# Optimization experiments

Hardware: AMD Instinct MI355X
Metric: run time of the kernel (lower is better)

Reference implementation:

```python
import jax, jax.numpy as jnp
import numpy as np

N = 4096      # nodes
IN = 512      # in_features
H = 8         # heads
D = 64        # out_features // heads (out % heads == 0)
EDGE_PROB = 0.01


def setup_inputs() -> dict:
    key = jax.random.key(0)
    kx, ka, kw, ko, kd = jax.random.split(key, 5)
    x = jax.random.normal(kx, (N, IN), dtype=jnp.float32)
    # dense binary adjacency with self-loops (original indexes adj[loc, :] as a mask)
    adj = (jax.random.uniform(ka, (N, N)) < EDGE_PROB).astype(jnp.float32)
    adj = jnp.maximum(adj, jnp.eye(N, dtype=jnp.float32))
    # stacked per-head params (original keeps Python lists of equal-sized heads)
    W = jax.random.normal(kw, (H, IN, D), dtype=jnp.float32) * (1.0 / np.sqrt(IN))
    a_origin = jax.random.normal(ko, (H, D), dtype=jnp.float32) * 0.1
    a_dst = jax.random.normal(kd, (H, D), dtype=jnp.float32) * 0.1
    return {"x": x, "adj": adj, "W": W, "a_origin": a_origin, "a_dst": a_dst}


def reference(x, adj, W, a_origin, a_dst):
    # per-head projection: mx[h] = x @ W[h]  -> [H, N, D]
    mx = jnp.einsum('nf,hfd->hnd', x, W)
    # clacAttn: e_ij = exp(mx_i . a_origin + mx_j . a_dst), masked by adj[i,:], row-normalised
    s_i = jnp.einsum('hnd,hd->hn', mx, a_origin)   # source term (row)
    t_j = jnp.einsum('hnd,hd->hn', mx, a_dst)      # dest term (col)
    logits = s_i[:, :, None] + t_j[:, None, :]     # [H, N, N]
    neg_inf = jnp.finfo(logits.dtype).min
    masked = jnp.where(adj[None] > 0, logits, neg_inf)
    attn = jax.nn.softmax(masked, axis=-1)         # == exp/masked-sum of original
    out_h = jnp.einsum('hij,hjd->hid', attn, mx)   # [H, N, D]
    # hstack over heads -> [N, H*D]
    return jnp.transpose(out_h, (1, 0, 2)).reshape(N, H * D)
```

## Files before the change

kernel.cpp:

```cpp
#include <hip/hip_runtime.h>
#include <hip/hip_bf16.h>

#define N_NODES 4096
#define IN_F    512
#define HEADS   8
#define DH      64
#define HD      512

typedef __bf16 bf16x8 __attribute__((ext_vector_type(8)));
typedef float  f32x4  __attribute__((ext_vector_type(4)));

__device__ __forceinline__ float bf_lo(unsigned u) { return __uint_as_float(u << 16); }
__device__ __forceinline__ float bf_hi(unsigned u) { return __uint_as_float(u & 0xffff0000u); }

#define KP 72

__global__ __launch_bounds__(256, 2) void k1_gemm(const float* __restrict__ X,
                                                  const float* __restrict__ W,
                                                  const float* __restrict__ a_dst,
                                                  __bf16* __restrict__ C,
                                                  float* __restrict__ et) {
    __shared__ __bf16 As[2][64][KP];
    __shared__ __bf16 Bs[2][64][KP];
    __shared__ float  ts[2][64];
    int tid  = threadIdx.x;
    int h    = blockIdx.x & 7;
    int y    = blockIdx.x >> 3;
    int row0 = y * 64, col0 = h * 64;
    int wave = tid >> 6, lane = tid & 63;
    int wm = wave >> 1, wn = wave & 1;
    int lr = lane & 15, kg = lane >> 4;

    f32x4 acc[2][2] = {};

    int sr = tid >> 3, sc = (tid & 7) * 8;
    const float* aptr0 = X + (size_t)(row0 + sr) * IN_F + sc;
    const float* aptr1 = aptr0 + (size_t)32 * IN_F;
    int dcol = tid & 63, fq = (tid >> 6) * 16;
    const float* wptr = W + ((size_t)h * IN_F + fq) * DH + dcol;

    f32x4 pa00 = *(const f32x4*)aptr0, pa01 = *(const f32x4*)(aptr0 + 4);
    f32x4 pa10 = *(const f32x4*)aptr1, pa11 = *(const f32x4*)(aptr1 + 4);
    float wv[16];
    #pragma unroll
    for (int i = 0; i < 16; ++i) wv[i] = wptr[(size_t)i * DH];

    float ad0 = a_dst[h * DH + wn * 32 + lr];
    float ad1 = a_dst[h * DH + wn * 32 + 16 + lr];

    #pragma unroll
    for (int k = 0; k < IN_F / 64; ++k) {
        int cur = k & 1;
        bf16x8 a0 = { (__bf16)pa00[0], (__bf16)pa00[1], (__bf16)pa00[2], (__bf16)pa00[3],
                      (__bf16)pa01[0], (__bf16)pa01[1], (__bf16)pa01[2], (__bf16)pa01[3] };
        bf16x8 a1 = { (__bf16)pa10[0], (__bf16)pa10[1], (__bf16)pa10[2], (__bf16)pa10[3],
                      (__bf16)pa11[0], (__bf16)pa11[1], (__bf16)pa11[2], (__bf16)pa11[3] };
        bf16x8 b0 = { (__bf16)wv[0],  (__bf16)wv[1],  (__bf16)wv[2],  (__bf16)wv[3],
                      (__bf16)wv[4],  (__bf16)wv[5],  (__bf16)wv[6],  (__bf16)wv[7] };
        bf16x8 b1 = { (__bf16)wv[8],  (__bf16)wv[9],  (__bf16)wv[10], (__bf16)wv[11],
                      (__bf16)wv[12], (__bf16)wv[13], (__bf16)wv[14], (__bf16)wv[15] };
        *(bf16x8*)&As[cur][sr][sc]        = a0;
        *(bf16x8*)&As[cur][sr + 32][sc]   = a1;
        *(bf16x8*)&Bs[cur][dcol][fq]      = b0;
        *(bf16x8*)&Bs[cur][dcol][fq + 8]  = b1;
        if (k + 1 < IN_F / 64) {
            int off = (k + 1) * 64;
            pa00 = *(const f32x4*)(aptr0 + off); pa01 = *(const f32x4*)(aptr0 + off + 4);
            pa10 = *(const f32x4*)(aptr1 + off); pa11 = *(const f32x4*)(aptr1 + off + 4);
            const float* wp = wptr + (size_t)off * DH;
            #pragma unroll
            for (int i = 0; i < 16; ++i) wv[i] = wp[(size_t)i * DH];
        }
        __syncthreads();
        #pragma unroll
        for (int kc = 0; kc < 2; ++kc) {
            bf16x8 af0 = *(const bf16x8*)&As[cur][wm * 32 + lr]     [kc * 32 + kg * 8];
            bf16x8 af1 = *(const bf16x8*)&As[cur][wm * 32 + 16 + lr][kc * 32 + kg * 8];
            bf16x8 bf0 = *(const bf16x8*)&Bs[cur][wn * 32 + lr]     [kc * 32 + kg * 8];
            bf16x8 bf1 = *(const bf16x8*)&Bs[cur][wn * 32 + 16 + lr][kc * 32 + kg * 8];
            acc[0][0] = __builtin_amdgcn_mfma_f32_16x16x32_bf16(af0, bf0, acc[0][0], 0, 0, 0);
            acc[0][1] = __builtin_amdgcn_mfma_f32_16x16x32_bf16(af0, bf1, acc[0][1], 0, 0, 0);
            acc[1][0] = __builtin_amdgcn_mfma_f32_16x16x32_bf16(af1, bf0, acc[1][0], 0, 0, 0);
            acc[1][1] = __builtin_amdgcn_mfma_f32_16x16x32_bf16(af1, bf1, acc[1][1], 0, 0, 0);
        }
    }

    #pragma unroll
    for (int mt = 0; mt < 2; ++mt) {
        #pragma unroll
        for (int nt = 0; nt < 2; ++nt) {
            int col = col0 + wn * 32 + nt * 16 + lr;
            #pragma unroll
            for (int r = 0; r < 4; ++r) {
                int row = row0 + wm * 32 + mt * 16 + kg * 4 + r;
                C[(size_t)row * HD + col] = (__bf16)acc[mt][nt][r];
            }
        }
    }
    #pragma unroll
    for (int mt = 0; mt < 2; ++mt) {
        #pragma unroll
        for (int r = 0; r < 4; ++r) {
            float p = ad0 * acc[mt][0][r] + ad1 * acc[mt][1][r];
            p += __shfl_xor(p, 1);
            p += __shfl_xor(p, 2);
            p += __shfl_xor(p, 4);
            p += __shfl_xor(p, 8);
            if (lr == 0) ts[wn][wm * 32 + mt * 16 + kg * 4 + r] = p;
        }
    }
    __syncthreads();
    if (tid < 64) {
        float t = ts[0][tid] + ts[1][tid];
        et[(size_t)(row0 + tid) * HEADS + h] = __expf(t);
    }
}

#define MAXNBR 512
__global__ __launch_bounds__(256) void k3_aggr(const float* __restrict__ adj,
                                               const __bf16* __restrict__ mx,
                                               const float* __restrict__ et,
                                               float* __restrict__ out) {
    __shared__ int   jlist[MAXNBR];
    __shared__ int   cnt;
    __shared__ float red[3][64][9];
    int tid  = threadIdx.x;
    int i    = blockIdx.x;
    int w    = tid >> 6, lane = tid & 63;
    if (tid == 0) cnt = 0;

    const uint4* arow = (const uint4*)(adj + (size_t)i * N_NODES);
    uint4 v0 = arow[tid];
    uint4 v1 = arow[256 + tid];
    uint4 v2 = arow[512 + tid];
    uint4 v3 = arow[768 + tid];
    int n = (v0.x != 0) + (v0.y != 0) + (v0.z != 0) + (v0.w != 0)
          + (v1.x != 0) + (v1.y != 0) + (v1.z != 0) + (v1.w != 0)
          + (v2.x != 0) + (v2.y != 0) + (v2.z != 0) + (v2.w != 0)
          + (v3.x != 0) + (v3.y != 0) + (v3.z != 0) + (v3.w != 0);
    __syncthreads();

    int pre = n;
    #pragma unroll
    for (int dlt = 1; dlt < 64; dlt <<= 1) {
        int t = __shfl_up(pre, dlt, 64);
        if (lane >= dlt) pre += t;
    }
    int wtot = __shfl(pre, 63, 64);
    int base = 0;
    if (lane == 63) base = atomicAdd(&cnt, wtot);
    base = __shfl(base, 63, 64);
    if (base + wtot <= MAXNBR) {
        int p_ = base + pre - n;
        int jb = tid * 4;
        if (v0.x) jlist[p_++] = jb;
        if (v0.y) jlist[p_++] = jb + 1;
        if (v0.z) jlist[p_++] = jb + 2;
        if (v0.w) jlist[p_++] = jb + 3;
        jb += 1024;
        if (v1.x) jlist[p_++] = jb;
        if (v1.y) jlist[p_++] = jb + 1;
        if (v1.z) jlist[p_++] = jb + 2;
        if (v1.w) jlist[p_++] = jb + 3;
        jb += 1024;
        if (v2.x) jlist[p_++] = jb;
        if (v2.y) jlist[p_++] = jb + 1;
        if (v2.z) jlist[p_++] = jb + 2;
        if (v2.w) jlist[p_++] = jb + 3;
        jb += 1024;
        if (v3.x) jlist[p_++] = jb;
        if (v3.y) jlist[p_++] = jb + 1;
        if (v3.z) jlist[p_++] = jb + 2;
        if (v3.w) jlist[p_++] = jb + 3;
    }
    __syncthreads();
    int c = cnt;
    if (c > MAXNBR) c = MAXNBR;

    int h = lane >> 3;
    const uint4* mxv = (const uint4*)mx;
    float acc[8] = {0.f, 0.f, 0.f, 0.f, 0.f, 0.f, 0.f, 0.f};
    float d = 0.f;

    int  k    = w;
    bool more = (k < c);
    int  j    = more ? jlist[k] : 0;
    float e   = 0.f;
    uint4 p   = {0u, 0u, 0u, 0u};
    if (more) {
        e = et[j * HEADS + h];
        p = mxv[(size_t)j * 64 + lane];
    }
    while (more) {
        int  k2   = k + 4;
        bool m2   = (k2 < c);
        int  j2   = m2 ? jlist[k2] : 0;
        float e2  = 0.f;
        uint4 p2  = {0u, 0u, 0u, 0u};
        if (m2) {
            e2 = et[j2 * HEADS + h];
            p2 = mxv[(size_t)j2 * 64 + lane];
        }
        acc[0] += e * bf_lo(p.x);  acc[1] += e * bf_hi(p.x);
        acc[2] += e * bf_lo(p.y);  acc[3] += e * bf_hi(p.y);
        acc[4] += e * bf_lo(p.z);  acc[5] += e * bf_hi(p.z);
        acc[6] += e * bf_lo(p.w);  acc[7] += e * bf_hi(p.w);
        d += e;
        k = k2; more = m2; j = j2; e = e2; p = p2;
    }

    if (w > 0) {
        #pragma unroll
        for (int q = 0; q < 8; ++q) red[w - 1][lane][q] = acc[q];
        red[w - 1][lane][8] = d;
    }
    __syncthreads();
    if (w == 0) {
        #pragma unroll
        for (int g = 0; g < 3; ++g) {
            #pragma unroll
            for (int q = 0; q < 8; ++q) acc[q] += red[g][lane][q];
            d += red[g][lane][8];
        }
        float inv = 1.f / d;
        f32x4 o0 = { acc[0] * inv, acc[1] * inv, acc[2] * inv, acc[3] * inv };
        f32x4 o1 = { acc[4] * inv, acc[5] * inv, acc[6] * inv, acc[7] * inv };
        float* orow = out + (size_t)i * HD + lane * 8;
        *(f32x4*)orow       = o0;
        *(f32x4*)(orow + 4) = o1;
    }
}

extern "C" void kernel_launch(void* const* d_in, const int* in_sizes, int n_in,
                              void* d_out, int out_size, void* d_ws, size_t ws_size,
                              hipStream_t stream) {
    const float* x     = (const float*)d_in[0];
    const float* adj   = (const float*)d_in[1];
    const float* W     = (const float*)d_in[2];
    const float* a_dst = (const float*)d_in[4];
    float* out = (float*)d_out;

    char* ws = (char*)d_ws;
    __bf16* mx = (__bf16*)ws;
    float*  et = (float*)(ws + 4194304);

    k1_gemm<<<dim3(512), dim3(256), 0, stream>>>(x, W, a_dst, mx, et);
    k3_aggr<<<dim3(N_NODES), dim3(256), 0, stream>>>(adj, mx, et, out);
}
```

Baseline: 127.9 us.

## Split adjacency scan into separate kernel and use single-wave gather blocks

```diff
diff --git a/kernel.cpp b/kernel.cpp
--- a/kernel.cpp
+++ b/kernel.cpp
@@ -13,120 +13,16 @@
 __device__ __forceinline__ float bf_lo(unsigned u) { return __uint_as_float(u << 16); }
 __device__ __forceinline__ float bf_hi(unsigned u) { return __uint_as_float(u & 0xffff0000u); }
 
-#define KP 72
-
-__global__ __launch_bounds__(256, 2) void k1_gemm(const float* __restrict__ X,
-                                                  const float* __restrict__ W,
-                                                  const float* __restrict__ a_dst,
-                                                  __bf16* __restrict__ C,
-                                                  float* __restrict__ et) {
-    __shared__ __bf16 As[2][64][KP];
-    __shared__ __bf16 Bs[2][64][KP];
-    __shared__ float  ts[2][64];
-    int tid  = threadIdx.x;
-    int h    = blockIdx.x & 7;
-    int y    = blockIdx.x >> 3;
-    int row0 = y * 64, col0 = h * 64;
-    int wave = tid >> 6, lane = tid & 63;
-    int wm = wave >> 1, wn = wave & 1;
-    int lr = lane & 15, kg = lane >> 4;
-
-    f32x4 acc[2][2] = {};
-
-    int sr = tid >> 3, sc = (tid & 7) * 8;
-    const float* aptr0 = X + (size_t)(row0 + sr) * IN_F + sc;
-    const float* aptr1 = aptr0 + (size_t)32 * IN_F;
-    int dcol = tid & 63, fq = (tid >> 6) * 16;
-    const float* wptr = W + ((size_t)h * IN_F + fq) * DH + dcol;
-
-    f32x4 pa00 = *(const f32x4*)aptr0, pa01 = *(const f32x4*)(aptr0 + 4);
-    f32x4 pa10 = *(const f32x4*)aptr1, pa11 = *(const f32x4*)(aptr1 + 4);
-    float wv[16];
-    #pragma unroll
-    for (int i = 0; i < 16; ++i) wv[i] = wptr[(size_t)i * DH];
-
-    float ad0 = a_dst[h * DH + wn * 32 + lr];
-    float ad1 = a_dst[h * DH + wn * 32 + 16 + lr];
-
-    #pragma unroll
-    for (int k = 0; k < IN_F / 64; ++k) {
-        int cur = k & 1;
-        bf16x8 a0 = { (__bf16)pa00[0], (__bf16)pa00[1], (__bf16)pa00[2], (__bf16)pa00[3],
-                      (__bf16)pa01[0], (__bf16)pa01[1], (__bf16)pa01[2], (__bf16)pa01[3] };
-        bf16x8 a1 = { (__bf16)pa10[0], (__bf16)pa10[1], (__bf16)pa10[2], (__bf16)pa10[3],
-                      (__bf16)pa11[0], (__bf16)pa11[1], (__bf16)pa11[2], (__bf16)pa11[3] };
-        bf16x8 b0 = { (__bf16)wv[0],  (__bf16)wv[1],  (__bf16)wv[2],  (__bf16)wv[3],
-                      (__bf16)wv[4],  (__bf16)wv[5],  (__bf16)wv[6],  (__bf16)wv[7] };
-        bf16x8 b1 = { (__bf16)wv[8],  (__bf16)wv[9],  (__bf16)wv[10], (__bf16)wv[11],
-                      (__bf16)wv[12], (__bf16)wv[13], (__bf16)wv[14], (__bf16)wv[15] };
-        *(bf16x8*)&As[cur][sr][sc]        = a0;
-        *(bf16x8*)&As[cur][sr + 32][sc]   = a1;
-        *(bf16x8*)&Bs[cur][dcol][fq]      = b0;
-        *(bf16x8*)&Bs[cur][dcol][fq + 8]  = b1;
-        if (k + 1 < IN_F / 64) {
-            int off = (k + 1) * 64;
-            pa00 = *(const f32x4*)(aptr0 + off); pa01 = *(const f32x4*)(aptr0 + off + 4);
-            pa10 = *(const f32x4*)(aptr1 + off); pa11 = *(const f32x4*)(aptr1 + off + 4);
-            const float* wp = wptr + (size_t)off * DH;
-            #pragma unroll
-            for (int i = 0; i < 16; ++i) wv[i] = wp[(size_t)i * DH];
-        }
-        __syncthreads();
-        #pragma unroll
-        for (int kc = 0; kc < 2; ++kc) {
-            bf16x8 af0 = *(const bf16x8*)&As[cur][wm * 32 + lr]     [kc * 32 + kg * 8];
-            bf16x8 af1 = *(const bf16x8*)&As[cur][wm * 32 + 16 + lr][kc * 32 + kg * 8];
-            bf16x8 bf0 = *(const bf16x8*)&Bs[cur][wn * 32 + lr]     [kc * 32 + kg * 8];
-            bf16x8 bf1 = *(const bf16x8*)&Bs[cur][wn * 32 + 16 + lr][kc * 32 + kg * 8];
-            acc[0][0] = __builtin_amdgcn_mfma_f32_16x16x32_bf16(af0, bf0, acc[0][0], 0, 0, 0);
-            acc[0][1] = __builtin_amdgcn_mfma_f32_16x16x32_bf16(af0, bf1, acc[0][1], 0, 0, 0);
-            acc[1][0] = __builtin_amdgcn_mfma_f32_16x16x32_bf16(af1, bf0, acc[1][0], 0, 0, 0);
-            acc[1][1] = __builtin_amdgcn_mfma_f32_16x16x32_bf16(af1, bf1, acc[1][1], 0, 0, 0);
-        }
-    }
-
-    #pragma unroll
-    for (int mt = 0; mt < 2; ++mt) {
-        #pragma unroll
-        for (int nt = 0; nt < 2; ++nt) {
-            int col = col0 + wn * 32 + nt * 16 + lr;
-            #pragma unroll
-            for (int r = 0; r < 4; ++r) {
-                int row = row0 + wm * 32 + mt * 16 + kg * 4 + r;
-                C[(size_t)row * HD + col] = (__bf16)acc[mt][nt][r];
-            }
-        }
-    }
-    #pragma unroll
-    for (int mt = 0; mt < 2; ++mt) {
-        #pragma unroll
-        for (int r = 0; r < 4; ++r) {
-            float p = ad0 * acc[mt][0][r] + ad1 * acc[mt][1][r];
-            p += __shfl_xor(p, 1);
-            p += __shfl_xor(p, 2);
-            p += __shfl_xor(p, 4);
-            p += __shfl_xor(p, 8);
-            if (lr == 0) ts[wn][wm * 32 + mt * 16 + kg * 4 + r] = p;
-        }
-    }
-    __syncthreads();
-    if (tid < 64) {
-        float t = ts[0][tid] + ts[1][tid];
-        et[(size_t)(row0 + tid) * HEADS + h] = __expf(t);
-    }
-}
-
 #define MAXNBR 512
-__global__ __launch_bounds__(256) void k3_aggr(const float* __restrict__ adj,
-                                               const __bf16* __restrict__ mx,
-                                               const float* __restrict__ et,
-                                               float* __restrict__ out) {
-    __shared__ int   jlist[MAXNBR];
-    __shared__ int   cnt;
-    __shared__ float red[3][64][9];
-    int tid  = threadIdx.x;
-    int i    = blockIdx.x;
-    int w    = tid >> 6, lane = tid & 63;
+#define JCAP   128
+__global__ __launch_bounds__(256) void k2_scan(const float* __restrict__ adj,
+                                               int* __restrict__ deg,
+                                               int* __restrict__ jl) {
+    __shared__ int jlist[MAXNBR];
+    __shared__ int cnt;
+    int tid = threadIdx.x;
+    int i   = blockIdx.x;
+    int lane = tid & 63;
     if (tid == 0) cnt = 0;
 
     const uint4* arow = (const uint4*)(adj + (size_t)i * N_NODES);
@@ -175,60 +71,155 @@
     }
     __syncthreads();
     int c = cnt;
-    if (c > MAXNBR) c = MAXNBR;
-
-    int h = lane >> 3;
-    const uint4* mxv = (const uint4*)mx;
-    float acc[8] = {0.f, 0.f, 0.f, 0.f, 0.f, 0.f, 0.f, 0.f};
-    float d = 0.f;
-
-    int  k    = w;
-    bool more = (k < c);
-    int  j    = more ? jlist[k] : 0;
-    float e   = 0.f;
-    uint4 p   = {0u, 0u, 0u, 0u};
-    if (more) {
-        e = et[j * HEADS + h];
-        p = mxv[(size_t)j * 64 + lane];
-    }
-    while (more) {
-        int  k2   = k + 4;
-        bool m2   = (k2 < c);
-        int  j2   = m2 ? jlist[k2] : 0;
-        float e2  = 0.f;
-        uint4 p2  = {0u, 0u, 0u, 0u};
-        if (m2) {
-            e2 = et[j2 * HEADS + h];
-            p2 = mxv[(size_t)j2 * 64 + lane];
-        }
-        acc[0] += e * bf_lo(p.x);  acc[1] += e * bf_hi(p.x);
-        acc[2] += e * bf_lo(p.y);  acc[3] += e * bf_hi(p.y);
-        acc[4] += e * bf_lo(p.z);  acc[5] += e * bf_hi(p.z);
-        acc[6] += e * bf_lo(p.w);  acc[7] += e * bf_hi(p.w);
-        d += e;
-        k = k2; more = m2; j = j2; e = e2; p = p2;
-    }
-
-    if (w > 0) {
+    if (c > JCAP) c = JCAP;
+    for (int t = tid; t < c; t += 256) jl[(size_t)i * JCAP + t] = jlist[t];
+    if (tid == 0) deg[i] = c;
+}
+
+#define KP 72
+
+__global__ __launch_bounds__(256, 2) void k1_gemm(const float* __restrict__ X,
+                                                  const float* __restrict__ W,
+                                                  const float* __restrict__ a_dst,
+                                                  __bf16* __restrict__ C,
+                                                  float* __restrict__ et) {
+    __shared__ __bf16 As[2][64][KP];
+    __shared__ __bf16 Bs[2][64][KP];
+    __shared__ float  ts[2][64];
+    int tid  = threadIdx.x;
+    int h    = blockIdx.x & 7;
+    int y    = blockIdx.x >> 3;
+    int row0 = y * 64, col0 = h * 64;
+    int wave = tid >> 6, lane = tid & 63;
+    int wm = wave >> 1, wn = wave & 1;
+    int lr = lane & 15, kg = lane >> 4;
+
+    f32x4 acc[2][2] = {};
+
+    int sr = tid >> 3, sc = (tid & 7) * 8;
+    const float* aptr0 = X + (size_t)(row0 + sr) * IN_F + sc;
+    const float* aptr1 = aptr0 + (size_t)32 * IN_F;
+    int dcol = tid & 63, fq = (tid >> 6) * 16;
+    const float* wptr = W + ((size_t)h * IN_F + fq) * DH + dcol;
+
+    f32x4 pa00 = *(const f32x4*)aptr0, pa01 = *(const f32x4*)(aptr0 + 4);
+    f32x4 pa10 = *(const f32x4*)aptr1, pa11 = *(const f32x4*)(aptr1 + 4);
+    float wv[16];
+    #pragma unroll
+    for (int i = 0; i < 16; ++i) wv[i] = wptr[(size_t)i * DH];
+
+    float ad0 = a_dst[h * DH + wn * 32 + lr];
+    float ad1 = a_dst[h * DH + wn * 32 + 16 + lr];
+
+    #pragma unroll
+    for (int k = 0; k < IN_F / 64; ++k) {
+        int cur = k & 1;
+        bf16x8 a0 = { (__bf16)pa00[0], (__bf16)pa00[1], (__bf16)pa00[2], (__bf16)pa00[3],
+                      (__bf16)pa01[0], (__bf16)pa01[1], (__bf16)pa01[2], (__bf16)pa01[3] };
+        bf16x8 a1 = { (__bf16)pa10[0], (__bf16)pa10[1], (__bf16)pa10[2], (__bf16)pa10[3],
+                      (__bf16)pa11[0], (__bf16)pa11[1], (__bf16)pa11[2], (__bf16)pa11[3] };
+        bf16x8 b0 = { (__bf16)wv[0],  (__bf16)wv[1],  (__bf16)wv[2],  (__bf16)wv[3],
+                      (__bf16)wv[4],  (__bf16)wv[5],  (__bf16)wv[6],  (__bf16)wv[7] };
+        bf16x8 b1 = { (__bf16)wv[8],  (__bf16)wv[9],  (__bf16)wv[10], (__bf16)wv[11],
+                      (__bf16)wv[12], (__bf16)wv[13], (__bf16)wv[14], (__bf16)wv[15] };
+        *(bf16x8*)&As[cur][sr][sc]        = a0;
+        *(bf16x8*)&As[cur][sr + 32][sc]   = a1;
+        *(bf16x8*)&Bs[cur][dcol][fq]      = b0;
+        *(bf16x8*)&Bs[cur][dcol][fq + 8]  = b1;
+        if (k + 1 < IN_F / 64) {
+            int off = (k + 1) * 64;
+            pa00 = *(const f32x4*)(aptr0 + off); pa01 = *(const f32x4*)(aptr0 + off + 4);
+            pa10 = *(const f32x4*)(aptr1 + off); pa11 = *(const f32x4*)(aptr1 + off + 4);
+            const float* wp = wptr + (size_t)off * DH;
+            #pragma unroll
+            for (int i = 0; i < 16; ++i) wv[i] = wp[(size_t)i * DH];
+        }
+        __syncthreads();
         #pragma unroll
-        for (int q = 0; q < 8; ++q) red[w - 1][lane][q] = acc[q];
-        red[w - 1][lane][8] = d;
+        for (int kc = 0; kc < 2; ++kc) {
+            bf16x8 af0 = *(const bf16x8*)&As[cur][wm * 32 + lr]     [kc * 32 + kg * 8];
+            bf16x8 af1 = *(const bf16x8*)&As[cur][wm * 32 + 16 + lr][kc * 32 + kg * 8];
+            bf16x8 bf0 = *(const bf16x8*)&Bs[cur][wn * 32 + lr]     [kc * 32 + kg * 8];
+            bf16x8 bf1 = *(const bf16x8*)&Bs[cur][wn * 32 + 16 + lr][kc * 32 + kg * 8];
+            acc[0][0] = __builtin_amdgcn_mfma_f32_16x16x32_bf16(af0, bf0, acc[0][0], 0, 0, 0);
+            acc[0][1] = __builtin_amdgcn_mfma_f32_16x16x32_bf16(af0, bf1, acc[0][1], 0, 0, 0);
+            acc[1][0] = __builtin_amdgcn_mfma_f32_16x16x32_bf16(af1, bf0, acc[1][0], 0, 0, 0);
+            acc[1][1] = __builtin_amdgcn_mfma_f32_16x16x32_bf16(af1, bf1, acc[1][1], 0, 0, 0);
+        }
+    }
+
+    #pragma unroll
+    for (int mt = 0; mt < 2; ++mt) {
+        #pragma unroll
+        for (int nt = 0; nt < 2; ++nt) {
+            int col = col0 + wn * 32 + nt * 16 + lr;
+            #pragma unroll
+            for (int r = 0; r < 4; ++r) {
+                int row = row0 + wm * 32 + mt * 16 + kg * 4 + r;
+                C[(size_t)row * HD + col] = (__bf16)acc[mt][nt][r];
+            }
+        }
+    }
+    #pragma unroll
+    for (int mt = 0; mt < 2; ++mt) {
+        #pragma unroll
+        for (int r = 0; r < 4; ++r) {
+            float p = ad0 * acc[mt][0][r] + ad1 * acc[mt][1][r];
+            p += __shfl_xor(p, 1);
+            p += __shfl_xor(p, 2);
+            p += __shfl_xor(p, 4);
+            p += __shfl_xor(p, 8);
+            if (lr == 0) ts[wn][wm * 32 + mt * 16 + kg * 4 + r] = p;
+        }
     }
     __syncthreads();
-    if (w == 0) {
-        #pragma unroll
-        for (int g = 0; g < 3; ++g) {
-            #pragma unroll
-            for (int q = 0; q < 8; ++q) acc[q] += red[g][lane][q];
-            d += red[g][lane][8];
-        }
-        float inv = 1.f / d;
-        f32x4 o0 = { acc[0] * inv, acc[1] * inv, acc[2] * inv, acc[3] * inv };
-        f32x4 o1 = { acc[4] * inv, acc[5] * inv, acc[6] * inv, acc[7] * inv };
-        float* orow = out + (size_t)i * HD + lane * 8;
-        *(f32x4*)orow       = o0;
-        *(f32x4*)(orow + 4) = o1;
-    }
+    if (tid < 64) {
+        float t = ts[0][tid] + ts[1][tid];
+        et[(size_t)(row0 + tid) * HEADS + h] = __expf(t);
+    }
+}
+
+__global__ __launch_bounds__(64) void k3_gather(const int* __restrict__ deg,
+                                                const int* __restrict__ jl,
+                                                const __bf16* __restrict__ mx,
+                                                const float* __restrict__ et,
+                                                float* __restrict__ out) {
+    int b    = blockIdx.x;
+    int s    = b & 1;
+    int i    = b >> 1;
+    int lane = threadIdx.x;
+    int c    = deg[i];
+
+    const int* row = jl + (size_t)i * JCAP;
+    int r0 = (lane      < c) ? row[lane]      : 0;
+    int r1 = (lane + 64 < c) ? row[lane + 64] : 0;
+
+    int hh = s * 4 + (lane >> 4);
+    const __bf16* mxp = mx + s * 256 + lane * 4;
+
+    float a0 = 0.f, a1 = 0.f, a2 = 0.f, a3 = 0.f, d = 0.f;
+
+    int   j = __shfl(r0, 0, 64);
+    float e = et[j * HEADS + hh];
+    uint2 v = *(const uint2*)(mxp + (size_t)j * HD);
+
+    for (int k = 0; k < c; ++k) {
+        int   k2 = k + 1;
+        int   j2 = 0; float e2 = 0.f; uint2 v2 = {0u, 0u};
+        if (k2 < c) {
+            j2 = __shfl(k2 < 64 ? r0 : r1, k2 & 63, 64);
+            e2 = et[j2 * HEADS + hh];
+            v2 = *(const uint2*)(mxp + (size_t)j2 * HD);
+        }
+        a0 += e * bf_lo(v.x);  a1 += e * bf_hi(v.x);
+        a2 += e * bf_lo(v.y);  a3 += e * bf_hi(v.y);
+        d  += e;
+        j = j2; e = e2; v = v2;
+    }
+
+    float inv = 1.f / d;
+    f32x4 o = { a0 * inv, a1 * inv, a2 * inv, a3 * inv };
+    *(f32x4*)(out + (size_t)i * HD + s * 256 + lane * 4) = o;
 }
 
 extern "C" void kernel_launch(void* const* d_in, const int* in_sizes, int n_in,
@@ -241,9 +232,12 @@
     float* out = (float*)d_out;
 
     char* ws = (char*)d_ws;
-    __bf16* mx = (__bf16*)ws;
-    float*  et = (float*)(ws + 4194304);
-
-    k1_gemm<<<dim3(512), dim3(256), 0, stream>>>(x, W, a_dst, mx, et);
-    k3_aggr<<<dim3(N_NODES), dim3(256), 0, stream>>>(adj, mx, et, out);
-}
+    __bf16* mx  = (__bf16*)ws;
+    float*  et  = (float*)(ws + 4194304);
+    int*    deg = (int*)  (ws + 4325376);
+    int*    jl  = (int*)  (ws + 4341760);
+
+    k2_scan  <<<dim3(N_NODES),     dim3(256), 0, stream>>>(adj, deg, jl);
+    k1_gemm  <<<dim3(512),         dim3(256), 0, stream>>>(x, W, a_dst, mx, et);
+    k3_gather<<<dim3(N_NODES * 2), dim3(64),  0, stream>>>(deg, jl, mx, et, out);
+}
```

Result: slower. 138.0 us (+7.9%).
